# Optimization experiments

Hardware: AMD Instinct MI355X
Metric: run time of the kernel (lower is better)

Reference implementation:

```python
import jax, jax.numpy as jnp
import numpy as np

HID = 512
NUM_NODES = 100000
N_BATCH = 20000


def _gru_cell(x, h, W_ih, W_hh, b_ih, b_hh):
    # torch nn.GRU single-step cell; gate order r, z, n
    gi = x @ W_ih.T + b_ih            # [N, 3H]
    gh = h @ W_hh.T + b_hh            # [N, 3H]
    i_r, i_z, i_n = jnp.split(gi, 3, axis=-1)
    h_r, h_z, h_n = jnp.split(gh, 3, axis=-1)
    r = jax.nn.sigmoid(i_r + h_r)
    z = jax.nn.sigmoid(i_z + h_z)
    n = jnp.tanh(i_n + r * h_n)
    return (1.0 - z) * n + z * h


def setup_inputs() -> dict:
    key = jax.random.key(0)
    ks = jax.random.split(key, 12)
    s = 1.0 / np.sqrt(HID)
    inp = {
        'conv_emb': jax.random.normal(ks[0], (N_BATCH, HID), jnp.float32),
        'static_table': jax.random.normal(ks[1], (NUM_NODES, HID), jnp.float32),
        'dynamic_table': jax.random.normal(ks[2], (NUM_NODES, 2, HID), jnp.float32),
        'W_ih0': jax.random.normal(ks[3], (3 * HID, 2 * HID), jnp.float32) * s,
        'W_hh0': jax.random.normal(ks[4], (3 * HID, HID), jnp.float32) * s,
        'b_ih0': jax.random.normal(ks[5], (3 * HID,), jnp.float32) * s,
        'b_hh0': jax.random.normal(ks[6], (3 * HID,), jnp.float32) * s,
        'W_ih1': jax.random.normal(ks[7], (3 * HID, HID), jnp.float32) * s,
        'W_hh1': jax.random.normal(ks[8], (3 * HID, HID), jnp.float32) * s,
        'b_ih1': jax.random.normal(ks[9], (3 * HID,), jnp.float32) * s,
        'b_hh1': jax.random.normal(ks[10], (3 * HID,), jnp.float32) * s,
        'nids': jnp.arange(N_BATCH, dtype=jnp.int32),  # unique global node ids
    }
    return inp


def reference(conv_emb, static_table, dynamic_table,
              W_ih0, W_hh0, b_ih0, b_hh0,
              W_ih1, W_hh1, b_ih1, b_hh1, nids):
    # gather: static embeddings for batch nodes, concat with conv output
    x = jnp.concatenate([conv_emb, static_table[nids]], axis=-1)  # [N, 2H]
    h0 = dynamic_table[nids]                                      # [N, L, H]
    # single-step 2-layer GRU (seq_len == 1)
    h_new0 = _gru_cell(x, h0[:, 0], W_ih0, W_hh0, b_ih0, b_hh0)   # [N, H]
    h_new1 = _gru_cell(h_new0, h0[:, 1], W_ih1, W_hh1, b_ih1, b_hh1)
    hn = jnp.stack([h_new0, h_new1], axis=1)                      # [N, L, H]
    # scatter updated hidden states back into the persistent table
    updated_table = dynamic_table.at[nids].set(hn)                # [num_nodes, L, H]
    return updated_table
```

## Files before the change

### kernel.cpp

```cpp
#include <hip/hip_runtime.h>

#define NB 20000
#define NNODES 100000
#define MB2 79
#define MP2 (MB2*256)
#define NBITW 3125
#define MBG 157
#define NBN 16
#define NGEMM (MBG*NBN)

typedef unsigned short u16;
typedef __bf16 bf16x8 __attribute__((ext_vector_type(8)));
typedef float f32x4 __attribute__((ext_vector_type(4)));

__device__ __forceinline__ u16 f2bf(float f) {
  union { float f; unsigned u; } v; v.f = f;
  unsigned r = v.u + 0x7fffu + ((v.u >> 16) & 1u);
  return (u16)(r >> 16);
}
__device__ __forceinline__ float bf2f(u16 b) {
  union { unsigned u; float f; } v; v.u = ((unsigned)b) << 16;
  return v.f;
}

__global__ void prep_bt0i(const float* __restrict__ Wih, const float* __restrict__ Whh,
                          u16* __restrict__ Bt) {
  int idx = blockIdx.x * 256 + threadIdx.x;
  if (idx >= 2048 * 384) return;
  int jg = idx / 384;
  int k = (idx % 384) * 4;
  int j = jg >> 2, g = jg & 3;
  float4 v = make_float4(0.f, 0.f, 0.f, 0.f);
  if (g < 2) {
    int row = g * 512 + j;
    v = (k < 1024) ? *(const float4*)(Wih + (size_t)row * 1024 + k)
                   : *(const float4*)(Whh + (size_t)row * 512 + (k - 1024));
  } else if (g == 2) {
    if (k < 1024) v = *(const float4*)(Wih + (size_t)(1024 + j) * 1024 + k);
  } else {
    if (k >= 1024) v = *(const float4*)(Whh + (size_t)(1024 + j) * 512 + (k - 1024));
  }
  ushort4 b; b.x = f2bf(v.x); b.y = f2bf(v.y); b.z = f2bf(v.z); b.w = f2bf(v.w);
  *(ushort4*)(Bt + (size_t)jg * 1536 + k) = b;
}

__global__ void prep_bt1i(const float* __restrict__ Wih, const float* __restrict__ Whh,
                          u16* __restrict__ Bt) {
  int idx = blockIdx.x * 256 + threadIdx.x;
  if (idx >= 2048 * 256) return;
  int jg = idx / 256;
  int k = (idx % 256) * 4;
  int j = jg >> 2, g = jg & 3;
  float4 v = make_float4(0.f, 0.f, 0.f, 0.f);
  if (g < 2) {
    int row = g * 512 + j;
    v = (k < 512) ? *(const float4*)(Wih + (size_t)row * 512 + k)
                  : *(const float4*)(Whh + (size_t)row * 512 + (k - 512));
  } else if (g == 2) {
    if (k < 512) v = *(const float4*)(Wih + (size_t)(1024 + j) * 512 + k);
  } else {
    if (k >= 512) v = *(const float4*)(Whh + (size_t)(1024 + j) * 512 + (k - 512));
  }
  ushort4 b; b.x = f2bf(v.x); b.y = f2bf(v.y); b.z = f2bf(v.z); b.w = f2bf(v.w);
  *(ushort4*)(Bt + (size_t)jg * 1024 + k) = b;
}

__global__ void prep_a(const float* __restrict__ conv, const float* __restrict__ stat,
                       const float* __restrict__ dyn, const int* __restrict__ nids,
                       u16* __restrict__ A0, u16* __restrict__ A1) {
  int idx = blockIdx.x * 256 + threadIdx.x;
  int n = idx >> 9;
  int c = (idx & 511) * 4;
  if (n >= MP2) return;
  float4 v = make_float4(0.f, 0.f, 0.f, 0.f);
  if (n < NB) {
    size_t nid = (size_t)nids[n];
    if (c < 512)        v = *(const float4*)(conv + (size_t)n * 512 + c);
    else if (c < 1024)  v = *(const float4*)(stat + nid * 512 + (c - 512));
    else if (c < 1536)  v = *(const float4*)(dyn + nid * 1024 + (c - 1024));
    else                v = *(const float4*)(dyn + nid * 1024 + 512 + (c - 1536));
  }
  ushort4 b; b.x = f2bf(v.x); b.y = f2bf(v.y); b.z = f2bf(v.z); b.w = f2bf(v.w);
  if (c < 1536) *(ushort4*)(A0 + (size_t)n * 1536 + c) = b;
  else          *(ushort4*)(A1 + (size_t)n * 1024 + (c - 1024)) = b;
  if (n >= NB && c < 512) *(ushort4*)(A1 + (size_t)n * 1024 + c) = b;
}

__global__ void zero_bits(unsigned* __restrict__ bits) {
  int i = blockIdx.x * 256 + threadIdx.x;
  if (i < NBITW) bits[i] = 0;
}
__global__ void set_bits(const int* __restrict__ nids, unsigned* __restrict__ bits) {
  int i = blockIdx.x * 256 + threadIdx.x;
  if (i < NB) {
    int nid = nids[i];
    atomicOr(&bits[nid >> 5], 1u << (nid & 31));
  }
}

template <int K, int LAYER>
__global__ __launch_bounds__(256, 3)
void gemmh(const u16* __restrict__ A, const u16* __restrict__ Bt,
           const float* __restrict__ bih, const float* __restrict__ bhh,
           const u16* __restrict__ hsrc, int hstride, const int* __restrict__ nids,
           u16* __restrict__ a1out, float* __restrict__ out) {
  constexpr int NT = K / 32;
  __shared__ u16 S[8192];

  int bid = blockIdx.x;
  int gidx = (bid & 7) * (NGEMM / 8) + (bid >> 3);
  int bn = gidx / MBG;
  int bm = gidx - bn * MBG;

  int t = threadIdx.x;
  int lane = t & 63, w = t >> 6;
  int fr = lane & 15, fq = lane >> 4;
  int wr = w >> 1, wc = w & 1;

  const u16* Ap = A + (size_t)bm * 128 * K;
  const u16* Bp = Bt + (size_t)bn * 128 * K;

  int goff[4], gsel[4];
#pragma unroll
  for (int l = 0; l < 4; ++l) {
    int c = l * 256 + t;
    gsel[l] = c >> 9;
    int cm = c & 511;
    int pair = cm >> 3, s = cm & 7;
    int u = s ^ (pair & 7);
    goff[l] = (pair * 2 + (u & 1)) * K + (u >> 1) * 8;
  }

  int offA[4], offB[4];
#pragma unroll
  for (int mi = 0; mi < 4; ++mi)
    offA[mi] = (wr * 32 + mi * 8 + (fr >> 1)) * 128 +
               (((fq * 2 + (fr & 1)) ^ ((fr >> 1) & 7)) << 4);
#pragma unroll
  for (int nf = 0; nf < 4; ++nf)
    offB[nf] = 8192 + (wc * 32 + nf * 8 + (fr >> 1)) * 128 +
               (((fq * 2 + (fr & 1)) ^ ((fr >> 1) & 7)) << 4);

  f32x4 acc[4][4] = {};

  for (int kt = 0; kt < NT; ++kt) {
#pragma unroll
    for (int l = 0; l < 4; ++l) {
      const u16* g = (gsel[l] ? Bp : Ap) + goff[l] + kt * 32;
      __builtin_amdgcn_global_load_lds((const __attribute__((address_space(1))) void*)g,
                                       (__attribute__((address_space(3))) void*)
                                       ((char*)S + (l * 256 + t) * 16), 16, 0, 0);
    }
    __syncthreads();

    bf16x8 af[4], bv[4];
#pragma unroll
    for (int mi = 0; mi < 4; ++mi) af[mi] = *(const bf16x8*)((const char*)S + offA[mi]);
#pragma unroll
    for (int nf = 0; nf < 4; ++nf) bv[nf] = *(const bf16x8*)((const char*)S + offB[nf]);
#pragma unroll
    for (int mi = 0; mi < 4; ++mi)
#pragma unroll
      for (int nf = 0; nf < 4; ++nf)
        acc[mi][nf] = __builtin_amdgcn_mfma_f32_16x16x32_bf16(af[mi], bv[nf],
                                                              acc[mi][nf], 0, 0, 0);
    __syncthreads();
  }

  int gg = fr & 3, jj = fr >> 2;
  float bias[4];
#pragma unroll
  for (int nf = 0; nf < 4; ++nf) {
    int j = bn * 32 + wc * 16 + nf * 4 + jj;
    bias[nf] = (gg == 0) ? bih[j] + bhh[j]
             : (gg == 1) ? bih[512 + j] + bhh[512 + j]
             : (gg == 2) ? bih[1024 + j] : bhh[1024 + j];
  }
#pragma unroll
  for (int mi = 0; mi < 4; ++mi) {
    int row = bm * 128 + wr * 64 + mi * 16 + fq * 4 + gg;
#pragma unroll
    for (int nf = 0; nf < 4; ++nf) {
      float v[4], v1[4], v2[4];
#pragma unroll
      for (int r = 0; r < 4; ++r) v[r] = acc[mi][nf][r] + bias[nf];
#pragma unroll
      for (int i = 0; i < 4; ++i) {
        float o = __shfl_xor(v[i ^ 2], 2);
        v1[i] = ((i ^ gg) & 2) ? o : v[i];
      }
#pragma unroll
      for (int i = 0; i < 4; ++i) {
        float o = __shfl_xor(v1[i ^ 1], 1);
        v2[i] = ((i ^ gg) & 1) ? o : v1[i];
      }
      if (row < NB) {
        int j = bn * 32 + wc * 16 + nf * 4 + jj;
        float rr = 1.f / (1.f + __expf(-v2[0]));
        float zz = 1.f / (1.f + __expf(-v2[1]));
        float nn = tanhf(fmaf(rr, v2[3], v2[2]));
        float h = bf2f(hsrc[(size_t)row * hstride + j]);
        float hp = (1.f - zz) * nn + zz * h;
        if (LAYER == 0) a1out[(size_t)row * 1024 + j] = f2bf(hp);
        out[(size_t)nids[row] * 1024 + LAYER * 512 + j] = hp;
      }
    }
  }
}

__global__ void copy_skip(const float4* __restrict__ src, float4* __restrict__ dst,
                          const unsigned* __restrict__ bits) {
  const size_t total = (size_t)NNODES * 256;
  for (size_t i = (size_t)blockIdx.x * 256 + threadIdx.x; i < total;
       i += (size_t)gridDim.x * 256) {
    int row = (int)(i >> 8);
    if (!((bits[row >> 5] >> (row & 31)) & 1u)) {
      dst[i] = src[i];
    }
  }
}

extern "C" void kernel_launch(void* const* d_in, const int* in_sizes, int n_in,
                              void* d_out, int out_size, void* d_ws, size_t ws_size,
                              hipStream_t stream) {
  const float* conv = (const float*)d_in[0];
  const float* stat = (const float*)d_in[1];
  const float* dyn  = (const float*)d_in[2];
  const float* Wih0 = (const float*)d_in[3];
  const float* Whh0 = (const float*)d_in[4];
  const float* bih0 = (const float*)d_in[5];
  const float* bhh0 = (const float*)d_in[6];
  const float* Wih1 = (const float*)d_in[7];
  const float* Whh1 = (const float*)d_in[8];
  const float* bih1 = (const float*)d_in[9];
  const float* bhh1 = (const float*)d_in[10];
  const int*   nids = (const int*)d_in[11];
  float* out = (float*)d_out;

  char* ws = (char*)d_ws;
  u16* A0  = (u16*)ws;
  u16* A1  = (u16*)(ws + 62128128);
  u16* Bt0 = (u16*)(ws + 103546880);
  u16* Bt1 = (u16*)(ws + 109838336);
  unsigned* bits = (unsigned*)(ws + 114032640);

  zero_bits<<<(NBITW + 255) / 256, 256, 0, stream>>>(bits);
  set_bits<<<(NB + 255) / 256, 256, 0, stream>>>(nids, bits);
  prep_bt0i<<<3072, 256, 0, stream>>>(Wih0, Whh0, Bt0);
  prep_bt1i<<<2048, 256, 0, stream>>>(Wih1, Whh1, Bt1);
  prep_a<<<(MP2 * 512) / 256, 256, 0, stream>>>(conv, stat, dyn, nids, A0, A1);

  gemmh<1536, 0><<<NGEMM, 256, 0, stream>>>(A0, Bt0, bih0, bhh0,
                                            A0 + 1024, 1536, nids, A1, out);
  gemmh<1024, 1><<<NGEMM, 256, 0, stream>>>(A1, Bt1, bih1, bhh1,
                                            A1 + 512, 1024, nids, (u16*)nullptr, out);

  copy_skip<<<2048, 256, 0, stream>>>((const float4*)dyn, (float4*)out, bits);
}
```

Baseline: 547.9 us.

## Enlarge GEMM tiles to 256x256 with double-buffered LDS and K=64 stages

Replaces the 128x128 tile GEMM, which had 256 threads and a single LDS buffer, with a 256x256 tile using 512 threads, a 64-wide K step and double-buffered LDS. The next stage is prefetched while MFMAs run on the current one, and s_setprio raises priority during the MFMA block. The goal is more operand reuse per global load and hiding load latency behind compute. In exchange the grid has only 632 blocks, the LDS footprint reaches 128KB and register pressure rises, which may limit occupancy and cause tail imbalance on 256 CUs.

```diff
diff --git a/kernel.cpp b/kernel.cpp
--- a/kernel.cpp
+++ b/kernel.cpp
@@ -5,9 +5,7 @@
 #define MB2 79
 #define MP2 (MB2*256)
 #define NBITW 3125
-#define MBG 157
-#define NBN 16
-#define NGEMM (MBG*NBN)
+#define NGEMM (MB2*8)
 
 typedef unsigned short u16;
 typedef __bf16 bf16x8 __attribute__((ext_vector_type(8)));
@@ -99,71 +97,114 @@
 }
 
 template <int K, int LAYER>
-__global__ __launch_bounds__(256, 3)
-void gemmh(const u16* __restrict__ A, const u16* __restrict__ Bt,
+__global__ __launch_bounds__(512, 2)
+void gemmt(const u16* __restrict__ A, const u16* __restrict__ Bt,
            const float* __restrict__ bih, const float* __restrict__ bhh,
            const u16* __restrict__ hsrc, int hstride, const int* __restrict__ nids,
            u16* __restrict__ a1out, float* __restrict__ out) {
-  constexpr int NT = K / 32;
-  __shared__ u16 S[8192];
+  constexpr int NT = K / 64;
+  __shared__ u16 S[2][2][2][8192];
 
   int bid = blockIdx.x;
-  int gidx = (bid & 7) * (NGEMM / 8) + (bid >> 3);
-  int bn = gidx / MBG;
-  int bm = gidx - bn * MBG;
+  int bn = bid & 7, bm = bid >> 3;
 
   int t = threadIdx.x;
   int lane = t & 63, w = t >> 6;
   int fr = lane & 15, fq = lane >> 4;
-  int wr = w >> 1, wc = w & 1;
-
-  const u16* Ap = A + (size_t)bm * 128 * K;
-  const u16* Bp = Bt + (size_t)bn * 128 * K;
-
-  int goff[4], gsel[4];
-#pragma unroll
-  for (int l = 0; l < 4; ++l) {
-    int c = l * 256 + t;
-    gsel[l] = c >> 9;
-    int cm = c & 511;
-    int pair = cm >> 3, s = cm & 7;
-    int u = s ^ (pair & 7);
-    goff[l] = (pair * 2 + (u & 1)) * K + (u >> 1) * 8;
-  }
-
-  int offA[4], offB[4];
-#pragma unroll
-  for (int mi = 0; mi < 4; ++mi)
-    offA[mi] = (wr * 32 + mi * 8 + (fr >> 1)) * 128 +
-               (((fq * 2 + (fr & 1)) ^ ((fr >> 1) & 7)) << 4);
+  int wm = w >> 2, wn = w & 3;
+
+  const u16* Ap = A + (size_t)bm * 256 * K;
+  const u16* Bp = Bt + (size_t)bn * 256 * K;
+
+  int srow[2], skc[2];
+#pragma unroll
+  for (int l = 0; l < 2; ++l) {
+    int c = l * 512 + t;
+    int p = c >> 4, up = c & 15;
+    int u = up ^ ((p & 7) << 1);
+    srow[l] = (p << 1) | (u & 1);
+    skc[l] = u >> 1;
+  }
+  auto stage = [&](int kt) {
+    char* base = (char*)S + (size_t)(kt & 1) * 65536;
+#pragma unroll
+    for (int m = 0; m < 2; ++m)
+#pragma unroll
+      for (int h = 0; h < 2; ++h)
+#pragma unroll
+        for (int l = 0; l < 2; ++l) {
+          const u16* g = (m ? Bp : Ap) + (size_t)(h * 128 + srow[l]) * K + kt * 64 + skc[l] * 8;
+          __builtin_amdgcn_global_load_lds(
+              (const __attribute__((address_space(1))) void*)g,
+              (__attribute__((address_space(3))) void*)
+              (base + m * 32768 + h * 16384 + (l * 512 + t) * 16), 16, 0, 0);
+        }
+  };
+
+  int swz = (((fr >> 1) & 7) << 1);
+  int ub = ((fq << 1) | (fr & 1)) ^ swz;
+  int offA[4], offA2[4], offB[4];
+#pragma unroll
+  for (int mi = 0; mi < 4; ++mi) {
+    offA[mi]  = wm * 16384 + (mi * 8 + (fr >> 1)) * 256 + ub * 16;
+    offA2[mi] = wm * 16384 + ((mi + 4) * 8 + (fr >> 1)) * 256 + ub * 16;
+  }
 #pragma unroll
   for (int nf = 0; nf < 4; ++nf)
-    offB[nf] = 8192 + (wc * 32 + nf * 8 + (fr >> 1)) * 128 +
-               (((fq * 2 + (fr & 1)) ^ ((fr >> 1) & 7)) << 4);
-
-  f32x4 acc[4][4] = {};
+    offB[nf] = 32768 + (wn >> 1) * 16384 +
+               ((wn & 1) * 32 + nf * 8 + (fr >> 1)) * 256 + ub * 16;
+
+  f32x4 acc[8][4] = {};
+
+  stage(0);
+  __syncthreads();
 
   for (int kt = 0; kt < NT; ++kt) {
-#pragma unroll
-    for (int l = 0; l < 4; ++l) {
-      const u16* g = (gsel[l] ? Bp : Ap) + goff[l] + kt * 32;
-      __builtin_amdgcn_global_load_lds((const __attribute__((address_space(1))) void*)g,
-                                       (__attribute__((address_space(3))) void*)
-                                       ((char*)S + (l * 256 + t) * 16), 16, 0, 0);
-    }
-    __syncthreads();
-
-    bf16x8 af[4], bv[4];
-#pragma unroll
-    for (int mi = 0; mi < 4; ++mi) af[mi] = *(const bf16x8*)((const char*)S + offA[mi]);
-#pragma unroll
-    for (int nf = 0; nf < 4; ++nf) bv[nf] = *(const bf16x8*)((const char*)S + offB[nf]);
+    const char* sb = (const char*)S + (size_t)(kt & 1) * 65536;
+
+    bf16x8 a0[4], b0[4], a1v[4];
+#pragma unroll
+    for (int mi = 0; mi < 4; ++mi) a0[mi] = *(const bf16x8*)(sb + offA[mi]);
+#pragma unroll
+    for (int nf = 0; nf < 4; ++nf) b0[nf] = *(const bf16x8*)(sb + offB[nf]);
+
+    if (kt + 1 < NT) stage(kt + 1);
+
+    __builtin_amdgcn_s_setprio(1);
 #pragma unroll
     for (int mi = 0; mi < 4; ++mi)
 #pragma unroll
       for (int nf = 0; nf < 4; ++nf)
-        acc[mi][nf] = __builtin_amdgcn_mfma_f32_16x16x32_bf16(af[mi], bv[nf],
+        acc[mi][nf] = __builtin_amdgcn_mfma_f32_16x16x32_bf16(a0[mi], b0[nf],
                                                               acc[mi][nf], 0, 0, 0);
+#pragma unroll
+    for (int mi = 0; mi < 4; ++mi) a1v[mi] = *(const bf16x8*)(sb + offA2[mi]);
+#pragma unroll
+    for (int mi = 0; mi < 4; ++mi)
+#pragma unroll
+      for (int nf = 0; nf < 4; ++nf)
+        acc[mi + 4][nf] = __builtin_amdgcn_mfma_f32_16x16x32_bf16(a1v[mi], b0[nf],
+                                                                  acc[mi + 4][nf], 0, 0, 0);
+#pragma unroll
+    for (int mi = 0; mi < 4; ++mi) a0[mi] = *(const bf16x8*)(sb + (offA[mi] ^ 128));
+#pragma unroll
+    for (int nf = 0; nf < 4; ++nf) b0[nf] = *(const bf16x8*)(sb + (offB[nf] ^ 128));
+#pragma unroll
+    for (int mi = 0; mi < 4; ++mi)
+#pragma unroll
+      for (int nf = 0; nf < 4; ++nf)
+        acc[mi][nf] = __builtin_amdgcn_mfma_f32_16x16x32_bf16(a0[mi], b0[nf],
+                                                              acc[mi][nf], 0, 0, 0);
+#pragma unroll
+    for (int mi = 0; mi < 4; ++mi) a1v[mi] = *(const bf16x8*)(sb + (offA2[mi] ^ 128));
+#pragma unroll
+    for (int mi = 0; mi < 4; ++mi)
+#pragma unroll
+      for (int nf = 0; nf < 4; ++nf)
+        acc[mi + 4][nf] = __builtin_amdgcn_mfma_f32_16x16x32_bf16(a1v[mi], b0[nf],
+                                                                  acc[mi + 4][nf], 0, 0, 0);
+    __builtin_amdgcn_s_setprio(0);
+
     __syncthreads();
   }
 
@@ -171,14 +212,14 @@
   float bias[4];
 #pragma unroll
   for (int nf = 0; nf < 4; ++nf) {
-    int j = bn * 32 + wc * 16 + nf * 4 + jj;
+    int j = bn * 64 + wn * 16 + nf * 4 + jj;
     bias[nf] = (gg == 0) ? bih[j] + bhh[j]
              : (gg == 1) ? bih[512 + j] + bhh[512 + j]
              : (gg == 2) ? bih[1024 + j] : bhh[1024 + j];
   }
 #pragma unroll
-  for (int mi = 0; mi < 4; ++mi) {
-    int row = bm * 128 + wr * 64 + mi * 16 + fq * 4 + gg;
+  for (int mi = 0; mi < 8; ++mi) {
+    int row = bm * 256 + wm * 128 + mi * 16 + fq * 4 + gg;
 #pragma unroll
     for (int nf = 0; nf < 4; ++nf) {
       float v[4], v1[4], v2[4];
@@ -195,7 +236,7 @@
         v2[i] = ((i ^ gg) & 1) ? o : v1[i];
       }
       if (row < NB) {
-        int j = bn * 32 + wc * 16 + nf * 4 + jj;
+        int j = bn * 64 + wn * 16 + nf * 4 + jj;
         float rr = 1.f / (1.f + __expf(-v2[0]));
         float zz = 1.f / (1.f + __expf(-v2[1]));
         float nn = tanhf(fmaf(rr, v2[3], v2[2]));
@@ -250,9 +291,9 @@
   prep_bt1i<<<2048, 256, 0, stream>>>(Wih1, Whh1, Bt1);
   prep_a<<<(MP2 * 512) / 256, 256, 0, stream>>>(conv, stat, dyn, nids, A0, A1);
 
-  gemmh<1536, 0><<<NGEMM, 256, 0, stream>>>(A0, Bt0, bih0, bhh0,
+  gemmt<1536, 0><<<NGEMM, 512, 0, stream>>>(A0, Bt0, bih0, bhh0,
                                             A0 + 1024, 1536, nids, A1, out);
-  gemmh<1024, 1><<<NGEMM, 256, 0, stream>>>(A1, Bt1, bih1, bhh1,
+  gemmt<1024, 1><<<NGEMM, 512, 0, stream>>>(A1, Bt1, bih1, bhh1,
                                             A1 + 512, 1024, nids, (u16*)nullptr, out);
 
   copy_skip<<<2048, 256, 0, stream>>>((const float4*)dyn, (float4*)out, bits);
```

Result: faster. 498.0 us (-9.1%).
